# Performance work log

Hardware: AMD Instinct MI355X
Metric: run time of the kernel (lower is better)

Reference implementation:

```python
import jax, jax.numpy as jnp
import numpy as np

# SPU(x) = x^2 - 0.5 for x >= 0, sigmoid(-x) - 1 for x < 0 (networks.SPU)

def _spu(x):
    return jnp.where(x >= 0, x * x - 0.5, jax.nn.sigmoid(-x) - 1.0)


def _spu_grad(x):
    xc = jnp.clip(x, -50.0, 50.0)  # avoid cosh overflow; masked out anyway
    neg_grad = -0.5 / (jnp.cosh(xc) + 1.0)
    return jnp.where(x >= 0, 2.0 * x, jnp.where(x <= -50.0, 0.0, neg_grad))


def setup_inputs() -> dict:
    key = jax.random.key(0)
    k1, k2 = jax.random.split(key)
    bs, n = 64, 65536
    l = 3.0 * jax.random.normal(k1, (bs, n), dtype=jnp.float32)
    u = l + jax.random.uniform(k2, (bs, n), dtype=jnp.float32, minval=0.0, maxval=4.0)
    return {"l": l, "u": u}


def reference(l, u):
    # --- spu(l, u): per-element sound linear bounds lw*x+lb <= SPU(x) <= uw*x+ub ---
    sl = _spu(l)
    su = _spu(u)

    # chord between (l, spu(l)) and (u, spu(u))  [calc_line_between]
    a_lu = (su - sl) / (u - l + 1e-8)
    b_lu = sl - l * a_lu

    # tangent at midpoint  [spu_tangent_parametrised, t=0.5]
    mid = 0.5 * (l + u)
    a_t = _spu_grad(mid)
    b_t = _spu(mid) - a_t * mid

    neg = u < 0
    pos = (~neg) & (l > 0)
    mixed = (~neg) & (~pos)
    normal = mixed & (su > sl)   # spu_mixed_normal_u
    # small = mixed & ~normal   -> spu_mixed_small_u

    # mixed lower-bound candidates
    # c0: y = -0.5
    # c1: chord from l to 0: spu(0) = -0.5
    a1 = (-0.5 - sl) / (-l + 1e-8)
    b1 = sl - l * a1
    # c2: tangent at u/2 (midpoint of [0, u]) -- only for the normal_u case
    h = 0.5 * u
    a2 = _spu_grad(h)
    b2 = _spu(h) - a2 * h

    def area(a, b):
        # find_area_proxy: -(u-l)*(a*l+b + a*u+b)
        return -(u - l) * (a * (l + u) + 2.0 * b)

    ar0 = area(0.0, -0.5)
    ar1 = area(a1, b1)
    ar2 = jnp.where(normal, area(a2, b2), jnp.inf)  # small_u has only 2 candidates
    idx = jnp.argmin(jnp.stack([ar0, ar1, ar2], axis=0), axis=0)
    a_m = jnp.where(idx == 0, 0.0, jnp.where(idx == 1, a1, a2))
    b_m = jnp.where(idx == 0, -0.5, jnp.where(idx == 1, b1, b2))

    lw = jnp.where(neg, a_lu, jnp.where(pos, a_t, a_m))
    lb = jnp.where(neg, b_lu, jnp.where(pos, b_t, b_m))
    uw = jnp.where(neg, a_t, jnp.where(pos | normal, a_lu, 0.0))
    ub = jnp.where(neg, b_t, jnp.where(pos | normal, b_lu, sl))

    # --- backsubstitution into the input layer (prev.al = l, prev.au = u) ---
    # nal is diagonal (lw) + bias column (lb); substitute() with constant input
    # bounds reduces to selecting l for positive coeffs, u for non-positive.
    nl = lb + jnp.where(lw > 0, lw * l, lw * u)
    nu = ub + jnp.where(uw > 0, uw * u, uw * l)
    return nl, nu
```

## Files before the change

### kernel.cpp

```cpp
#include <hip/hip_runtime.h>
#include <math.h>

typedef float f32x4 __attribute__((ext_vector_type(4)));

__device__ __forceinline__ float frcp(float x) { return __builtin_amdgcn_rcpf(x); }

__device__ __forceinline__ void spu_bounds(float l, float u, float& nl, float& nu) {
    const float mid = 0.5f * (l + u);

    const float e_l = __expf(l);
    const float e_u = __expf(u);
    const float e_m = __expf(mid);
    const float r_l = frcp(1.0f + e_l);
    const float r_u = frcp(1.0f + e_u);
    const float r_m = frcp(1.0f + e_m);

    const float sl = (l   >= 0.0f) ? fmaf(l,   l,   -0.5f) : (r_l - 1.0f);
    const float su = (u   >= 0.0f) ? fmaf(u,   u,   -0.5f) : (r_u - 1.0f);
    const float sm = (mid >= 0.0f) ? fmaf(mid, mid, -0.5f) : (r_m - 1.0f);
    const float gm = (mid >= 0.0f) ? (2.0f * mid)
                   : ((mid <= -50.0f) ? 0.0f : (-e_m * r_m * r_m));

    const float a_lu = (su - sl) * frcp(u - l + 1e-8f);
    const float b_lu = sl - l * a_lu;

    const float a_t = gm;
    const float b_t = sm - gm * mid;

    const bool neg    = (u < 0.0f);
    const bool pos    = (!neg) && (l > 0.0f);
    const bool mixed  = (!neg) && (!pos);
    const bool normal = mixed && (su > sl);

    const float a1 = (-0.5f - sl) * frcp(1e-8f - l);
    const float b1 = sl - l * a1;
    const float a2 = u;
    const float b2 = -fmaf(0.25f * u, u, 0.5f);

    const float dlu = u - l;
    const float slu = u + l;
    const float ar0 = dlu;
    const float ar1 = -dlu * fmaf(a1, slu, 2.0f * b1);
    const float ar2 = normal ? (-dlu * fmaf(a2, slu, 2.0f * b2)) : INFINITY;

    int idx = 0;
    float best = ar0;
    if (ar1 < best) { best = ar1; idx = 1; }
    if (ar2 < best) { idx = 2; }
    const float a_m = (idx == 0) ? 0.0f  : ((idx == 1) ? a1 : a2);
    const float b_m = (idx == 0) ? -0.5f : ((idx == 1) ? b1 : b2);

    const float lw = neg ? a_lu : (pos ? a_t : a_m);
    const float lb = neg ? b_lu : (pos ? b_t : b_m);
    const float uw = neg ? a_t : ((pos || normal) ? a_lu : 0.0f);
    const float ub = neg ? b_t : ((pos || normal) ? b_lu : sl);

    nl = lb + ((lw > 0.0f) ? lw * l : lw * u);
    nu = ub + ((uw > 0.0f) ? uw * u : uw * l);
}

__device__ __forceinline__ void spu_bounds4(const f32x4 lv, const f32x4 uv,
                                            f32x4& a, f32x4& b) {
    float a0, b0, a1, b1, a2, b2, a3, b3;
    spu_bounds(lv.x, uv.x, a0, b0);
    spu_bounds(lv.y, uv.y, a1, b1);
    spu_bounds(lv.z, uv.z, a2, b2);
    spu_bounds(lv.w, uv.w, a3, b3);
    a.x = a0; a.y = a1; a.z = a2; a.w = a3;
    b.x = b0; b.y = b1; b.z = b2; b.w = b3;
}

__global__ void __launch_bounds__(256) spu_pointwise_kernel(
        const float* __restrict__ l, const float* __restrict__ u,
        float* __restrict__ out_nl, float* __restrict__ out_nu,
        int n4, int n) {
    const int tid = blockIdx.x * blockDim.x + threadIdx.x;
    const int stride = gridDim.x * blockDim.x;
    const int pairs = n4 >> 1;

    const f32x4* __restrict__ l4 = reinterpret_cast<const f32x4*>(l);
    const f32x4* __restrict__ u4 = reinterpret_cast<const f32x4*>(u);
    f32x4* __restrict__ nl4 = reinterpret_cast<f32x4*>(out_nl);
    f32x4* __restrict__ nu4 = reinterpret_cast<f32x4*>(out_nu);

    for (int i = tid; i < pairs; i += stride) {
        const int j = i + pairs;
        const f32x4 lv0 = __builtin_nontemporal_load(l4 + i);
        const f32x4 uv0 = __builtin_nontemporal_load(u4 + i);
        const f32x4 lv1 = __builtin_nontemporal_load(l4 + j);
        const f32x4 uv1 = __builtin_nontemporal_load(u4 + j);
        f32x4 a0, b0, a1, b1;
        spu_bounds4(lv0, uv0, a0, b0);
        spu_bounds4(lv1, uv1, a1, b1);
        __builtin_nontemporal_store(a0, nl4 + i);
        __builtin_nontemporal_store(b0, nu4 + i);
        __builtin_nontemporal_store(a1, nl4 + j);
        __builtin_nontemporal_store(b1, nu4 + j);
    }

    for (int i = 2 * pairs + tid; i < n4; i += stride) {
        const f32x4 lv = __builtin_nontemporal_load(l4 + i);
        const f32x4 uv = __builtin_nontemporal_load(u4 + i);
        f32x4 a, b;
        spu_bounds4(lv, uv, a, b);
        __builtin_nontemporal_store(a, nl4 + i);
        __builtin_nontemporal_store(b, nu4 + i);
    }

    for (int i = n4 * 4 + tid; i < n; i += stride) {
        spu_bounds(l[i], u[i], out_nl[i], out_nu[i]);
    }
}

extern "C" void kernel_launch(void* const* d_in, const int* in_sizes, int n_in,
                              void* d_out, int out_size, void* d_ws, size_t ws_size,
                              hipStream_t stream) {
    const float* l = (const float*)d_in[0];
    const float* u = (const float*)d_in[1];
    float* out = (float*)d_out;

    const int n = in_sizes[0];
    float* out_nl = out;
    float* out_nu = out + n;

    const int n4 = n / 4;
    const int pairs = n4 / 2;
    const int block = 256;
    int grid = (pairs + block - 1) / block;
    if (grid > 4096) grid = 4096;
    if (grid < 1) grid = 1;

    spu_pointwise_kernel<<<grid, block, 0, stream>>>(l, u, out_nl, out_nu, n4, n);
}
```

Baseline: 17.80 us.

## Simplify SPU bound arithmetic and use single-vector grid-stride loop

Rewrites the per-element math: the area comparisons are reduced algebraically to cheaper comparisons against constants, reciprocals are hoisted, multiply-adds are fused, and the lw/uw sign selection is replaced by fminf/fmaxf. The -50 clamp on the midpoint gradient is dropped, which relies on exp underflow giving zero. The kernel loop drops the two-vectors-per-thread pairing for one f32x4 per iteration, switches the loads from nontemporal to ordinary loads, and sizes the grid from n4, still capped at 4096 blocks. This aims to cut ALU work in a kernel that may be partly compute-bound, at the cost of less memory-level parallelism per thread.

After: 15.57 us. 12.5% less time.

```diff
diff --git a/kernel.cpp b/kernel.cpp
--- a/kernel.cpp
+++ b/kernel.cpp
@@ -7,6 +7,7 @@
 
 __device__ __forceinline__ void spu_bounds(float l, float u, float& nl, float& nu) {
     const float mid = 0.5f * (l + u);
+    const float dlu = u - l;
 
     const float e_l = __expf(l);
     const float e_u = __expf(u);
@@ -14,60 +15,45 @@
     const float r_l = frcp(1.0f + e_l);
     const float r_u = frcp(1.0f + e_u);
     const float r_m = frcp(1.0f + e_m);
+    const float rg  = frcp(dlu + 1e-8f);
+    const float rl0 = frcp(1e-8f - l);
 
     const float sl = (l   >= 0.0f) ? fmaf(l,   l,   -0.5f) : (r_l - 1.0f);
     const float su = (u   >= 0.0f) ? fmaf(u,   u,   -0.5f) : (r_u - 1.0f);
     const float sm = (mid >= 0.0f) ? fmaf(mid, mid, -0.5f) : (r_m - 1.0f);
-    const float gm = (mid >= 0.0f) ? (2.0f * mid)
-                   : ((mid <= -50.0f) ? 0.0f : (-e_m * r_m * r_m));
+    const float gm = (mid >= 0.0f) ? (mid + mid) : (-e_m * r_m * r_m);
 
-    const float a_lu = (su - sl) * frcp(u - l + 1e-8f);
-    const float b_lu = sl - l * a_lu;
-
-    const float a_t = gm;
-    const float b_t = sm - gm * mid;
+    const float a_lu = (su - sl) * rg;
+    const float b_lu = fmaf(-l, a_lu, sl);
+    const float b_t  = fmaf(-gm, mid, sm);
 
     const bool neg    = (u < 0.0f);
     const bool pos    = (!neg) && (l > 0.0f);
-    const bool mixed  = (!neg) && (!pos);
-    const bool normal = mixed && (su > sl);
+    const bool normal = (!neg) && (!pos) && (su > sl);
 
-    const float a1 = (-0.5f - sl) * frcp(1e-8f - l);
-    const float b1 = sl - l * a1;
-    const float a2 = u;
+    const float a1 = (-0.5f - sl) * rl0;
+    const float b1 = fmaf(-l, a1, sl);
     const float b2 = -fmaf(0.25f * u, u, 0.5f);
 
-    const float dlu = u - l;
-    const float slu = u + l;
-    const float ar0 = dlu;
-    const float ar1 = -dlu * fmaf(a1, slu, 2.0f * b1);
-    const float ar2 = normal ? (-dlu * fmaf(a2, slu, 2.0f * b2)) : INFINITY;
+    const float x1 = fmaf(a1, dlu, sl + sl);
+    const float x2 = fmaf(u, fmaf(0.5f, u, l), -1.0f);
 
-    int idx = 0;
-    float best = ar0;
-    if (ar1 < best) { best = ar1; idx = 1; }
-    if (ar2 < best) { idx = 2; }
-    const float a_m = (idx == 0) ? 0.0f  : ((idx == 1) ? a1 : a2);
-    const float b_m = (idx == 0) ? -0.5f : ((idx == 1) ? b1 : b2);
+    const bool  c1 = (x1 > -1.0f);
+    float am = c1 ? a1 : 0.0f;
+    float bm = c1 ? b1 : -0.5f;
+    const float xb = c1 ? x1 : -1.0f;
+    const bool  c2 = normal && (x2 > xb);
+    am = c2 ? u  : am;
+    bm = c2 ? b2 : bm;
 
-    const float lw = neg ? a_lu : (pos ? a_t : a_m);
-    const float lb = neg ? b_lu : (pos ? b_t : b_m);
-    const float uw = neg ? a_t : ((pos || normal) ? a_lu : 0.0f);
-    const float ub = neg ? b_t : ((pos || normal) ? b_lu : sl);
+    const float lw = neg ? a_lu : (pos ? gm  : am);
+    const float lb = neg ? b_lu : (pos ? b_t : bm);
+    const bool  uc = (!neg) && (pos || normal);
+    const float uw = neg ? gm  : (uc ? a_lu : 0.0f);
+    const float ub = neg ? b_t : (uc ? b_lu : sl);
 
-    nl = lb + ((lw > 0.0f) ? lw * l : lw * u);
-    nu = ub + ((uw > 0.0f) ? uw * u : uw * l);
-}
-
-__device__ __forceinline__ void spu_bounds4(const f32x4 lv, const f32x4 uv,
-                                            f32x4& a, f32x4& b) {
-    float a0, b0, a1, b1, a2, b2, a3, b3;
-    spu_bounds(lv.x, uv.x, a0, b0);
-    spu_bounds(lv.y, uv.y, a1, b1);
-    spu_bounds(lv.z, uv.z, a2, b2);
-    spu_bounds(lv.w, uv.w, a3, b3);
-    a.x = a0; a.y = a1; a.z = a2; a.w = a3;
-    b.x = b0; b.y = b1; b.z = b2; b.w = b3;
+    nl = lb + fminf(lw * l, lw * u);
+    nu = ub + fmaxf(uw * l, uw * u);
 }
 
 __global__ void __launch_bounds__(256) spu_pointwise_kernel(
@@ -76,33 +62,23 @@
         int n4, int n) {
     const int tid = blockIdx.x * blockDim.x + threadIdx.x;
     const int stride = gridDim.x * blockDim.x;
-    const int pairs = n4 >> 1;
 
     const f32x4* __restrict__ l4 = reinterpret_cast<const f32x4*>(l);
     const f32x4* __restrict__ u4 = reinterpret_cast<const f32x4*>(u);
     f32x4* __restrict__ nl4 = reinterpret_cast<f32x4*>(out_nl);
     f32x4* __restrict__ nu4 = reinterpret_cast<f32x4*>(out_nu);
 
-    for (int i = tid; i < pairs; i += stride) {
-        const int j = i + pairs;
-        const f32x4 lv0 = __builtin_nontemporal_load(l4 + i);
-        const f32x4 uv0 = __builtin_nontemporal_load(u4 + i);
-        const f32x4 lv1 = __builtin_nontemporal_load(l4 + j);
-        const f32x4 uv1 = __builtin_nontemporal_load(u4 + j);
-        f32x4 a0, b0, a1, b1;
-        spu_bounds4(lv0, uv0, a0, b0);
-        spu_bounds4(lv1, uv1, a1, b1);
-        __builtin_nontemporal_store(a0, nl4 + i);
-        __builtin_nontemporal_store(b0, nu4 + i);
-        __builtin_nontemporal_store(a1, nl4 + j);
-        __builtin_nontemporal_store(b1, nu4 + j);
-    }
-
-    for (int i = 2 * pairs + tid; i < n4; i += stride) {
-        const f32x4 lv = __builtin_nontemporal_load(l4 + i);
-        const f32x4 uv = __builtin_nontemporal_load(u4 + i);
+    for (int i = tid; i < n4; i += stride) {
+        const f32x4 lv = l4[i];
+        const f32x4 uv = u4[i];
+        float a0, b0, a1, b1, a2, b2, a3, b3;
+        spu_bounds(lv.x, uv.x, a0, b0);
+        spu_bounds(lv.y, uv.y, a1, b1);
+        spu_bounds(lv.z, uv.z, a2, b2);
+        spu_bounds(lv.w, uv.w, a3, b3);
         f32x4 a, b;
-        spu_bounds4(lv, uv, a, b);
+        a.x = a0; a.y = a1; a.z = a2; a.w = a3;
+        b.x = b0; b.y = b1; b.z = b2; b.w = b3;
         __builtin_nontemporal_store(a, nl4 + i);
         __builtin_nontemporal_store(b, nu4 + i);
     }
@@ -124,9 +100,8 @@
     float* out_nu = out + n;
 
     const int n4 = n / 4;
-    const int pairs = n4 / 2;
     const int block = 256;
-    int grid = (pairs + block - 1) / block;
+    int grid = (n4 + block - 1) / block;
     if (grid > 4096) grid = 4096;
     if (grid < 1) grid = 1;
 
```
